# Kernel optimization log

Measured on AMD Instinct MI355X. Metric: run time of the kernel, lower is better.

The kernel has to match this reference:

```python
import jax, jax.numpy as jnp
import numpy as np

NEG_BIG = -9e15
LRELU_SLOPE = 0.2  # alpha

N = 8192
IN_F = 256
OUT_F = 128


def setup_inputs() -> dict:
    key = jax.random.key(0)
    k1, k2, k3, k4 = jax.random.split(key, 4)
    inputs = jax.random.normal(k1, (N, IN_F), dtype=jnp.float32)
    adj = jax.random.randint(k2, (N, N), 0, 2, dtype=jnp.int32)
    # xavier_uniform with gain=1.414
    gain = 1.414
    bW = gain * np.sqrt(6.0 / (IN_F + OUT_F))
    W = jax.random.uniform(k3, (IN_F, OUT_F), minval=-bW, maxval=bW, dtype=jnp.float32)
    ba = gain * np.sqrt(6.0 / (2 * OUT_F + 1))
    a = jax.random.uniform(k4, (2 * OUT_F, 1), minval=-ba, maxval=ba, dtype=jnp.float32)
    return {"inputs": inputs, "adj": adj, "W": W, "a": a}


def reference(inputs, adj, W, a):
    # h: [N, F']
    h = inputs @ W
    # a^T [h_i || h_j] = h_i . a[:F'] + h_j . a[F':]  -- avoids the O(N^2 * 2F') concat
    a1 = a[:OUT_F, 0]   # [F']
    a2 = a[OUT_F:, 0]   # [F']
    s1 = h @ a1         # [N]
    s2 = h @ a2         # [N]
    e = s1[:, None] + s2[None, :]                      # [N, N]
    e = jnp.where(e >= 0, e, LRELU_SLOPE * e)          # LeakyReLU(alpha)
    scores = jnp.where(adj > 0, e, jnp.float32(NEG_BIG))
    attention = jax.nn.softmax(scores, axis=1)         # row softmax; dropout p=0
    h_prime = attention @ h                            # [N, F']
    return jax.nn.elu(h_prime)                         # concat=True -> elu
```

## Files before the change

### kernel.cpp

```cpp
#include <hip/hip_runtime.h>
#include <hip/hip_bf16.h>

#define NN   8192
#define INF_ 256
#define OUTF 128
#define SLOPE 0.2f
#define NJC  4
#define JCHUNK (NN / NJC)
#define NT   (JCHUNK / 128)

typedef float f32x4  __attribute__((ext_vector_type(4)));
typedef float f32x16 __attribute__((ext_vector_type(16)));
typedef short bf16x8 __attribute__((ext_vector_type(8)));
typedef int   i32x4  __attribute__((ext_vector_type(4)));
typedef unsigned short u16;
typedef u16 u16x4 __attribute__((ext_vector_type(4)));

__device__ __forceinline__ u16 f2bf(float f) {
  return __builtin_bit_cast(u16, __float2bfloat16(f));
}

__global__ __launch_bounds__(256) void gat_k1(
    const float* __restrict__ X, const float* __restrict__ W,
    const float* __restrict__ a, u16* __restrict__ hbF,
    float* __restrict__ s1, float* __restrict__ s2) {
  __shared__ float xs[32 * INF_];
  const int t = threadIdx.x;
  const int r0 = blockIdx.x * 32;
  {
    const f32x4* src = (const f32x4*)(X + (size_t)r0 * INF_);
    f32x4* dst = (f32x4*)xs;
    for (int i = t; i < 32 * INF_ / 4; i += 256) dst[i] = src[i];
  }
  __syncthreads();
  const int cg = t & 31;
  const int rg = t >> 5;
  float acc[4][4];
#pragma unroll
  for (int i = 0; i < 4; i++)
#pragma unroll
    for (int j = 0; j < 4; j++) acc[i][j] = 0.f;

  for (int k = 0; k < INF_; k += 4) {
    f32x4 xv[4];
#pragma unroll
    for (int i = 0; i < 4; i++) xv[i] = *(const f32x4*)&xs[(rg * 4 + i) * INF_ + k];
#pragma unroll
    for (int kk = 0; kk < 4; kk++) {
      f32x4 wv = *(const f32x4*)&W[(k + kk) * OUTF + cg * 4];
#pragma unroll
      for (int i = 0; i < 4; i++)
#pragma unroll
        for (int j = 0; j < 4; j++) acc[i][j] = fmaf(xv[i][kk], wv[j], acc[i][j]);
    }
  }

  f32x4 a1v = *(const f32x4*)&a[cg * 4];
  f32x4 a2v = *(const f32x4*)&a[OUTF + cg * 4];
  float p1[4], p2[4];
#pragma unroll
  for (int i = 0; i < 4; i++) {
    p1[i] = acc[i][0] * a1v[0] + acc[i][1] * a1v[1] + acc[i][2] * a1v[2] + acc[i][3] * a1v[3];
    p2[i] = acc[i][0] * a2v[0] + acc[i][1] * a2v[1] + acc[i][2] * a2v[2] + acc[i][3] * a2v[3];
  }
#pragma unroll
  for (int m = 1; m < 32; m <<= 1) {
#pragma unroll
    for (int i = 0; i < 4; i++) {
      p1[i] += __shfl_xor(p1[i], m);
      p2[i] += __shfl_xor(p2[i], m);
    }
  }
  if (cg == 0) {
#pragma unroll
    for (int i = 0; i < 4; i++) {
      s1[r0 + rg * 4 + i] = p1[i];
      s2[r0 + rg * 4 + i] = p2[i];
    }
  }

  const int R0 = r0 + rg * 4;
  const int J  = R0 >> 4;
  const int gg = (R0 >> 3) & 1;
  const int e0 = R0 & 7;
#pragma unroll
  for (int j = 0; j < 4; j++) {
    const int C = cg * 4 + j;
    u16x4 pk;
#pragma unroll
    for (int i = 0; i < 4; i++) pk[i] = f2bf(acc[i][j]);
    size_t flat = ((size_t)(J * 4 + (C >> 5)) * 64 + (C & 31) + 32 * gg) * 8 + e0;
    *(u16x4*)(hbF + flat) = pk;
  }
}

__global__ __launch_bounds__(256) void gat_k2(const float* __restrict__ s2,
                                              float* __restrict__ s2m) {
  __shared__ float sm[4];
  const int t = threadIdx.x;
  float m = -1e30f;
  for (int i = t; i < NN; i += 256) m = fmaxf(m, s2[i]);
#pragma unroll
  for (int k = 1; k < 64; k <<= 1) m = fmaxf(m, __shfl_xor(m, k));
  if ((t & 63) == 0) sm[t >> 6] = m;
  __syncthreads();
  if (t == 0) *s2m = fmaxf(fmaxf(sm[0], sm[1]), fmaxf(sm[2], sm[3]));
}

__device__ __forceinline__ void st16(float* dst, const f32x16& A, int g) {
#pragma unroll
  for (int r = 0; r < 16; r++) {
    const int dr = (r & 3) + 8 * (r >> 2) + 4 * g;
    dst[dr * 128] = A[r];
  }
}
__device__ __forceinline__ void ad16(float* dst, const f32x16& A, int g) {
#pragma unroll
  for (int r = 0; r < 16; r++) {
    const int dr = (r & 3) + 8 * (r >> 2) + 4 * g;
    dst[dr * 128] += A[r];
  }
}

__global__ __launch_bounds__(512, 4) void gat_k3(
    const int* __restrict__ adj, const u16* __restrict__ hbF,
    const float* __restrict__ s1g, const float* __restrict__ s2g,
    const float* __restrict__ s2maxp, float* __restrict__ part,
    float* __restrict__ dpart) {
  __shared__ int adjs[2 * 4096];
  __shared__ float dred[256];
  const int t = threadIdx.x;
  const int w = t >> 6;
  const int l = t & 63;
  const int rb = blockIdx.x & 255;
  const int jc = blockIdx.x >> 8;
  const int r0 = rb * 32;
  const int j0 = jc * JCHUNK;
  const int row = l & 31;
  const int g = l >> 5;

  const float s1r = s1g[r0 + row];
  const float s2m = *s2maxp;
  float Mi = s1r + s2m;
  Mi = fmaxf(Mi, SLOPE * Mi);

  f32x16 acc0 = 0.f, acc1 = 0.f, acc2 = 0.f, acc3 = 0.f;

  const int srow = t >> 4;
  const int scg = t & 15;
  const int cA = 4 * scg + ((srow & 1) ? 64 : 0);
  const int cB = 4 * scg + ((srow & 1) ? 0 : 64);
  const int slotA = ((cA >> 2) ^ srow) & 31;
  const int slotB = ((cB >> 2) ^ srow) & 31;
  const int* gsrc = adj + (size_t)(r0 + srow) * NN + j0;

  i32x4 stA, stB;
#define STAGE_LOAD(TL)                              \
  {                                                 \
    const int* p_ = gsrc + 128 * (TL);              \
    stA = *(const i32x4*)(p_ + cA);                 \
    stB = *(const i32x4*)(p_ + cB);                 \
  }
#define STAGE_WRITE(BUF)                            \
  {                                                 \
    int* b_ = &adjs[(BUF) * 4096 + srow * 128];     \
    *(i32x4*)(b_ + slotA * 4) = stA;                \
    *(i32x4*)(b_ + slotB * 4) = stB;                \
  }

  const int c0 = 16 * w + 8 * g;
  const int sl0 = (((c0 >> 2) + 0) ^ row) & 31;
  const int sl1 = (((c0 >> 2) + 1) ^ row) & 31;

  const bf16x8* bp = (const bf16x8*)hbF;
  const float* s2b = s2g + j0;
  float dsum = 0.f;

  STAGE_LOAD(0);
  STAGE_WRITE(0);
  STAGE_LOAD(1);
  __syncthreads();

  int cur = 0;
  for (int tt = 0; tt < NT; tt++) {
    const int n = jc * 128 + 8 * tt + w;
    const bf16x8* bq = bp + (size_t)(n * 4) * 64 + l;
    bf16x8 b0 = bq[0], b1 = bq[64], b2 = bq[128], b3 = bq[192];

    const int* abuf = &adjs[cur * 4096 + row * 128];
    i32x4 A0 = *(const i32x4*)(abuf + sl0 * 4);
    i32x4 A1 = *(const i32x4*)(abuf + sl1 * 4);
    f32x4 s0  = *(const f32x4*)(s2b + 128 * tt + c0);
    f32x4 s1v = *(const f32x4*)(s2b + 128 * tt + c0 + 4);

    bf16x8 af;
#pragma unroll
    for (int e = 0; e < 8; e++) {
      float x = s1r + ((e < 4) ? s0[e] : s1v[e - 4]);
      x = fmaxf(x, SLOPE * x);
      float p = __expf(x - Mi);
      const int ad = (e < 4) ? A0[e] : A1[e - 4];
      p = (ad > 0) ? p : 0.f;
      dsum += p;
      af[e] = (short)f2bf(p);
    }
    acc0 = __builtin_amdgcn_mfma_f32_32x32x16_bf16(af, b0, acc0, 0, 0, 0);
    acc1 = __builtin_amdgcn_mfma_f32_32x32x16_bf16(af, b1, acc1, 0, 0, 0);
    acc2 = __builtin_amdgcn_mfma_f32_32x32x16_bf16(af, b2, acc2, 0, 0, 0);
    acc3 = __builtin_amdgcn_mfma_f32_32x32x16_bf16(af, b3, acc3, 0, 0, 0);

    if (tt + 1 < NT) STAGE_WRITE(cur ^ 1);
    if (tt + 2 < NT) STAGE_LOAD(tt + 2);
    __syncthreads();
    cur ^= 1;
  }

  dsum += __shfl_xor(dsum, 32);
  if (l < 32) dred[w * 32 + l] = dsum;

  float* lred = (float*)adjs;
  const int colw = l & 31;
  if (w < 2) {
    st16(&lred[w * 4096 + 0 * 32 + colw], acc0, g);
    st16(&lred[w * 4096 + 1 * 32 + colw], acc1, g);
    st16(&lred[w * 4096 + 2 * 32 + colw], acc2, g);
    st16(&lred[w * 4096 + 3 * 32 + colw], acc3, g);
  }
  __syncthreads();
  if (t < 32) {
    float d = 0.f;
#pragma unroll
    for (int w8 = 0; w8 < 8; w8++) d += dred[w8 * 32 + t];
    dpart[jc * NN + r0 + t] = d;
  }
  if (w == 2 || w == 3) {
    ad16(&lred[(w - 2) * 4096 + 0 * 32 + colw], acc0, g);
    ad16(&lred[(w - 2) * 4096 + 1 * 32 + colw], acc1, g);
    ad16(&lred[(w - 2) * 4096 + 2 * 32 + colw], acc2, g);
    ad16(&lred[(w - 2) * 4096 + 3 * 32 + colw], acc3, g);
  }
  __syncthreads();
  if (w == 4 || w == 5) {
    ad16(&lred[(w - 4) * 4096 + 0 * 32 + colw], acc0, g);
    ad16(&lred[(w - 4) * 4096 + 1 * 32 + colw], acc1, g);
    ad16(&lred[(w - 4) * 4096 + 2 * 32 + colw], acc2, g);
    ad16(&lred[(w - 4) * 4096 + 3 * 32 + colw], acc3, g);
  }
  __syncthreads();
  if (w == 6 || w == 7) {
    ad16(&lred[(w - 6) * 4096 + 0 * 32 + colw], acc0, g);
    ad16(&lred[(w - 6) * 4096 + 1 * 32 + colw], acc1, g);
    ad16(&lred[(w - 6) * 4096 + 2 * 32 + colw], acc2, g);
    ad16(&lred[(w - 6) * 4096 + 3 * 32 + colw], acc3, g);
  }
  __syncthreads();

  const int flat = t * 8;
  f32x4 pa = *(f32x4*)&lred[flat];
  f32x4 pb = *(f32x4*)&lred[flat + 4];
  pa += *(f32x4*)&lred[4096 + flat];
  pb += *(f32x4*)&lred[4096 + flat + 4];
  float* pp = part + (size_t)jc * (NN * OUTF) + (size_t)r0 * OUTF + flat;
  *(f32x4*)pp = pa;
  *(f32x4*)(pp + 4) = pb;
}

__global__ __launch_bounds__(256) void gat_k4(
    const float* __restrict__ part, const float* __restrict__ dpart,
    float* __restrict__ out) {
  const int idx = blockIdx.x * 256 + threadIdx.x;
  const int e4 = idx * 4;
  const int i = e4 >> 7;
  f32x4 p = {0.f, 0.f, 0.f, 0.f};
  float d = 0.f;
#pragma unroll
  for (int jc = 0; jc < NJC; jc++) {
    p += *(const f32x4*)&part[(size_t)jc * (NN * OUTF) + e4];
    d += dpart[jc * NN + i];
  }
  d = fmaxf(d, 1e-30f);
  f32x4 r;
#pragma unroll
  for (int k = 0; k < 4; k++) {
    float v = p[k] / d;
    r[k] = (v > 0.f) ? v : expm1f(v);
  }
  *(f32x4*)&out[e4] = r;
}

extern "C" void kernel_launch(void* const* d_in, const int* in_sizes, int n_in,
                              void* d_out, int out_size, void* d_ws, size_t ws_size,
                              hipStream_t stream) {
  (void)in_sizes; (void)n_in; (void)out_size; (void)ws_size;
  const float* X  = (const float*)d_in[0];
  const int*  adj = (const int*)d_in[1];
  const float* W  = (const float*)d_in[2];
  const float* a  = (const float*)d_in[3];
  float* out = (float*)d_out;

  char* ws = (char*)d_ws;
  u16*   hbF   = (u16*)ws;
  float* s1    = (float*)(ws + (2u << 20));
  float* s2    = (float*)(ws + (2u << 20) + (32u << 10));
  float* s2m   = (float*)(ws + (2u << 20) + (64u << 10));
  float* dpart = (float*)(ws + (2u << 20) + (128u << 10));
  float* part  = (float*)(ws + (4u << 20));

  gat_k1<<<NN / 32, 256, 0, stream>>>(X, W, a, hbF, s1, s2);
  gat_k2<<<1, 256, 0, stream>>>(s2, s2m);
  gat_k3<<<256 * NJC, 512, 0, stream>>>(adj, hbF, s1, s2, s2m, part, dpart);
  gat_k4<<<(NN * OUTF / 4) / 256, 256, 0, stream>>>(part, dpart, out);
}
```

Measured before the change: 110.1 us.

## Load adjacency directly from global memory, drop LDS staging and per-tile barriers

Removes the double-buffered LDS staging of adjacency tiles and the __syncthreads in the main loop. Each lane now reads its own 8 adjacency ints straight from global memory. The LeakyReLU and max-subtraction are folded into per-row constants, so each element costs one fmax of two fma-style terms. The gain is no barriers and less LDS traffic, but the direct global loads are less coalesced (32 rows, 32 bytes each per wave) and there is no explicit prefetch.

Result: slower. 139.7 us (+26.9%).

```diff
diff --git a/kernel.cpp b/kernel.cpp
--- a/kernel.cpp
+++ b/kernel.cpp
@@ -127,7 +127,7 @@
     const float* __restrict__ s1g, const float* __restrict__ s2g,
     const float* __restrict__ s2maxp, float* __restrict__ part,
     float* __restrict__ dpart) {
-  __shared__ int adjs[2 * 4096];
+  __shared__ float lred[8192];
   __shared__ float dred[256];
   const int t = threadIdx.x;
   const int w = t >> 6;
@@ -143,62 +143,31 @@
   const float s2m = *s2maxp;
   float Mi = s1r + s2m;
   Mi = fmaxf(Mi, SLOPE * Mi);
+  const float ar = s1r - Mi;
+  const float br = SLOPE * s1r - Mi;
 
   f32x16 acc0 = 0.f, acc1 = 0.f, acc2 = 0.f, acc3 = 0.f;
 
-  const int srow = t >> 4;
-  const int scg = t & 15;
-  const int cA = 4 * scg + ((srow & 1) ? 64 : 0);
-  const int cB = 4 * scg + ((srow & 1) ? 0 : 64);
-  const int slotA = ((cA >> 2) ^ srow) & 31;
-  const int slotB = ((cB >> 2) ^ srow) & 31;
-  const int* gsrc = adj + (size_t)(r0 + srow) * NN + j0;
-
-  i32x4 stA, stB;
-#define STAGE_LOAD(TL)                              \
-  {                                                 \
-    const int* p_ = gsrc + 128 * (TL);              \
-    stA = *(const i32x4*)(p_ + cA);                 \
-    stB = *(const i32x4*)(p_ + cB);                 \
-  }
-#define STAGE_WRITE(BUF)                            \
-  {                                                 \
-    int* b_ = &adjs[(BUF) * 4096 + srow * 128];     \
-    *(i32x4*)(b_ + slotA * 4) = stA;                \
-    *(i32x4*)(b_ + slotB * 4) = stB;                \
-  }
-
   const int c0 = 16 * w + 8 * g;
-  const int sl0 = (((c0 >> 2) + 0) ^ row) & 31;
-  const int sl1 = (((c0 >> 2) + 1) ^ row) & 31;
-
-  const bf16x8* bp = (const bf16x8*)hbF;
-  const float* s2b = s2g + j0;
+  const int*    ap = adj + (size_t)(r0 + row) * NN + j0 + c0;
+  const float*  sp = s2g + j0 + c0;
+  const bf16x8* bp = (const bf16x8*)hbF + ((size_t)(jc * 128 + w) * 4) * 64 + l;
+
   float dsum = 0.f;
-
-  STAGE_LOAD(0);
-  STAGE_WRITE(0);
-  STAGE_LOAD(1);
-  __syncthreads();
-
-  int cur = 0;
   for (int tt = 0; tt < NT; tt++) {
-    const int n = jc * 128 + 8 * tt + w;
-    const bf16x8* bq = bp + (size_t)(n * 4) * 64 + l;
+    i32x4 A0 = *(const i32x4*)(ap + 128 * tt);
+    i32x4 A1 = *(const i32x4*)(ap + 128 * tt + 4);
+    f32x4 s0  = *(const f32x4*)(sp + 128 * tt);
+    f32x4 s1v = *(const f32x4*)(sp + 128 * tt + 4);
+    const bf16x8* bq = bp + (size_t)tt * 8 * 4 * 64;
     bf16x8 b0 = bq[0], b1 = bq[64], b2 = bq[128], b3 = bq[192];
 
-    const int* abuf = &adjs[cur * 4096 + row * 128];
-    i32x4 A0 = *(const i32x4*)(abuf + sl0 * 4);
-    i32x4 A1 = *(const i32x4*)(abuf + sl1 * 4);
-    f32x4 s0  = *(const f32x4*)(s2b + 128 * tt + c0);
-    f32x4 s1v = *(const f32x4*)(s2b + 128 * tt + c0 + 4);
-
     bf16x8 af;
 #pragma unroll
     for (int e = 0; e < 8; e++) {
-      float x = s1r + ((e < 4) ? s0[e] : s1v[e - 4]);
-      x = fmaxf(x, SLOPE * x);
-      float p = __expf(x - Mi);
+      const float sv = (e < 4) ? s0[e] : s1v[e - 4];
+      const float y = fmaxf(ar + sv, fmaf(SLOPE, sv, br));
+      float p = __expf(y);
       const int ad = (e < 4) ? A0[e] : A1[e - 4];
       p = (ad > 0) ? p : 0.f;
       dsum += p;
@@ -208,17 +177,11 @@
     acc1 = __builtin_amdgcn_mfma_f32_32x32x16_bf16(af, b1, acc1, 0, 0, 0);
     acc2 = __builtin_amdgcn_mfma_f32_32x32x16_bf16(af, b2, acc2, 0, 0, 0);
     acc3 = __builtin_amdgcn_mfma_f32_32x32x16_bf16(af, b3, acc3, 0, 0, 0);
-
-    if (tt + 1 < NT) STAGE_WRITE(cur ^ 1);
-    if (tt + 2 < NT) STAGE_LOAD(tt + 2);
-    __syncthreads();
-    cur ^= 1;
   }
 
   dsum += __shfl_xor(dsum, 32);
   if (l < 32) dred[w * 32 + l] = dsum;
 
-  float* lred = (float*)adjs;
   const int colw = l & 31;
   if (w < 2) {
     st16(&lred[w * 4096 + 0 * 32 + colw], acc0, g);
```
